# Kernel optimization log

Measured on AMD Instinct MI355X. Metric: run time of the kernel, lower is better.

## Reference

```python
import jax, jax.numpy as jnp
import numpy as np

EMB_DIM = 768
HEADS = 12
HEAD_DIM = EMB_DIM // HEADS  # 64


def setup_inputs() -> dict:
    key = jax.random.key(0)
    ks = jax.random.split(key, 9)
    s = 1.0 / np.sqrt(EMB_DIM)
    d = dict(
        x=jax.random.normal(ks[0], (2, 2048, EMB_DIM), dtype=jnp.float32),
        wq_w=jax.random.normal(ks[1], (EMB_DIM, EMB_DIM), dtype=jnp.float32) * s,
        wq_b=jax.random.normal(ks[2], (EMB_DIM,), dtype=jnp.float32) * 0.01,
        wk_w=jax.random.normal(ks[3], (EMB_DIM, EMB_DIM), dtype=jnp.float32) * s,
        wk_b=jax.random.normal(ks[4], (EMB_DIM,), dtype=jnp.float32) * 0.01,
        wv_w=jax.random.normal(ks[5], (EMB_DIM, EMB_DIM), dtype=jnp.float32) * s,
        wv_b=jax.random.normal(ks[6], (EMB_DIM,), dtype=jnp.float32) * 0.01,
        wo_w=jax.random.normal(ks[7], (EMB_DIM, EMB_DIM), dtype=jnp.float32) * s,
        wo_b=jax.random.normal(ks[8], (EMB_DIM,), dtype=jnp.float32) * 0.01,
    )
    return d


def reference(x, wq_w, wq_b, wk_w, wk_b, wv_w, wv_b, wo_w, wo_b):
    b, n, _ = x.shape
    # Linear projections (torch Linear: x @ W^T + b). q scaled by 1/8 == 1/sqrt(head_dim).
    q = (x @ wq_w.T + wq_b) / 8.0
    k = x @ wk_w.T + wk_b
    v = x @ wv_w.T + wv_b
    # [b, h, n, d]
    q = q.reshape(b, n, HEADS, HEAD_DIM).transpose(0, 2, 1, 3)
    k = k.reshape(b, n, HEADS, HEAD_DIM).transpose(0, 2, 1, 3)
    v = v.reshape(b, n, HEADS, HEAD_DIM).transpose(0, 2, 1, 3)
    # Full [b, h, n, n] score matrix with causal mask (strict upper triangle = -inf)
    scores = jnp.einsum('bhqd,bhkd->bhqk', q, k)
    causal = jnp.tril(jnp.ones((n, n), dtype=bool))  # True where allowed
    scores = jnp.where(causal[None, None], scores, -jnp.inf)
    attn = jax.nn.softmax(scores, axis=-1)
    out = jnp.einsum('bhqk,bhkd->bhqd', attn, v)
    out = out.transpose(0, 2, 1, 3).reshape(b, n, EMB_DIM)
    return out @ wo_w.T + wo_b
```

## Files before the change

kernel.cpp:

```cpp
#include <hip/hip_runtime.h>
#include <hip/hip_bf16.h>
#include <math.h>

#define EMB  768
#define NH   12
#define HD   64
#define SEQ  2048
#define BATCH 2
#define NTOK 4096

typedef __attribute__((ext_vector_type(8))) short short8;
typedef __attribute__((ext_vector_type(4))) float float4v;

static __device__ __forceinline__ short f2bf(float f) {
    __hip_bfloat16 h = __float2bfloat16(f);
    return *reinterpret_cast<short*>(&h);
}

static __device__ __forceinline__ void gll16(const void* g, void* l) {
    __builtin_amdgcn_global_load_lds(
        (const __attribute__((address_space(1))) void*)g,
        (__attribute__((address_space(3))) void*)l, 16, 0, 0);
}

__global__ __launch_bounds__(256) void cast_kernel(
    const float* __restrict__ x,  const float* __restrict__ wq,
    const float* __restrict__ wk, const float* __restrict__ wv,
    const float* __restrict__ wo,
    __hip_bfloat16* __restrict__ xb,  __hip_bfloat16* __restrict__ wqb,
    __hip_bfloat16* __restrict__ wkb, __hip_bfloat16* __restrict__ wvb,
    __hip_bfloat16* __restrict__ wob)
{
    const size_t S0 = (size_t)NTOK * EMB;
    const size_t S1 = (size_t)EMB * EMB;
    size_t i = ((size_t)blockIdx.x * 256 + threadIdx.x) * 8;
    const float* src; __hip_bfloat16* dst; size_t off;
    if      (i < S0)            { src = x;  dst = xb;  off = i; }
    else if (i < S0 + S1)       { src = wq; dst = wqb; off = i - S0; }
    else if (i < S0 + 2 * S1)   { src = wk; dst = wkb; off = i - S0 - S1; }
    else if (i < S0 + 3 * S1)   { src = wv; dst = wvb; off = i - S0 - 2 * S1; }
    else                        { src = wo; dst = wob; off = i - S0 - 3 * S1; }
    float4 f0 = *(const float4*)&src[off];
    float4 f1 = *(const float4*)&src[off + 4];
    short8 o;
    o[0] = f2bf(f0.x); o[1] = f2bf(f0.y); o[2] = f2bf(f0.z); o[3] = f2bf(f0.w);
    o[4] = f2bf(f1.x); o[5] = f2bf(f1.y); o[6] = f2bf(f1.z); o[7] = f2bf(f1.w);
    *(short8*)&dst[off] = o;
}

__global__ __launch_bounds__(256) void qkv_mfma_kernel(
    const __hip_bfloat16* __restrict__ xb,
    const __hip_bfloat16* __restrict__ wqb, const float* __restrict__ bq,
    const __hip_bfloat16* __restrict__ wkb, const float* __restrict__ bk,
    const __hip_bfloat16* __restrict__ wvb, const float* __restrict__ bv,
    __hip_bfloat16* __restrict__ q, __hip_bfloat16* __restrict__ k,
    __hip_bfloat16* __restrict__ vT)
{
    __shared__ __align__(16) short SM[16384];
    short* As = SM;
    short* Bs = SM + 8192;
    const int t = threadIdx.x;
    const int w = t >> 6, lane = t & 63;
    const int col = lane & 15, quad = lane >> 4;
    const int wm = w >> 1, wn = w & 1;
    const int m0 = blockIdx.y * 128;
    const int mat = blockIdx.x / 6;
    const int jj0 = (blockIdx.x % 6) * 128;
    const short* X = (const short*)xb;
    const short* W = (const short*)((mat == 0) ? wqb : (mat == 1) ? wkb : wvb);
    const float* bias = (mat == 0) ? bq : (mat == 1) ? bk : bv;

    float4v acc[4][4];
    #pragma unroll
    for (int mi = 0; mi < 4; ++mi)
        #pragma unroll
        for (int ni = 0; ni < 4; ++ni) acc[mi][ni] = (float4v){0.f, 0.f, 0.f, 0.f};

    for (int kb = 0; kb < EMB; kb += 64) {
        #pragma unroll
        for (int c = 0; c < 4; ++c) {
            int I = w * 256 + c * 64 + lane;
            int row = I >> 3;
            int c8 = (I & 7) ^ (row & 7);
            gll16(X + (size_t)(m0 + row) * EMB + kb + c8 * 8,
                  &As[(w * 256 + c * 64) * 8]);
            gll16(W + (size_t)(jj0 + row) * EMB + kb + c8 * 8,
                  &Bs[(w * 256 + c * 64) * 8]);
        }
        __syncthreads();
        #pragma unroll
        for (int ks = 0; ks < 2; ++ks) {
            short8 a[4], b[4];
            #pragma unroll
            for (int mi = 0; mi < 4; ++mi) {
                int row = wm * 64 + mi * 16 + col;
                a[mi] = *(short8*)&As[row * 64 + (((ks * 4 + quad) ^ (row & 7)) * 8)];
            }
            #pragma unroll
            for (int ni = 0; ni < 4; ++ni) {
                int row = wn * 64 + ni * 16 + col;
                b[ni] = *(short8*)&Bs[row * 64 + (((ks * 4 + quad) ^ (row & 7)) * 8)];
            }
            #pragma unroll
            for (int mi = 0; mi < 4; ++mi)
                #pragma unroll
                for (int ni = 0; ni < 4; ++ni)
                    acc[mi][ni] = __builtin_amdgcn_mfma_f32_16x16x32_bf16(
                        a[mi], b[ni], acc[mi][ni], 0, 0, 0);
        }
        __syncthreads();
    }
    const int bi = m0 >> 11, n0g = m0 & (SEQ - 1);
    if (mat != 2) {
        const float scale = (mat == 0) ? 0.125f : 1.0f;
        __hip_bfloat16* dstqk = (mat == 0) ? q : k;
        #pragma unroll
        for (int mi = 0; mi < 4; ++mi) {
            #pragma unroll
            for (int ni = 0; ni < 4; ++ni) {
                int gj = jj0 + wn * 64 + ni * 16 + col;
                int h = gj >> 6, d = gj & 63;
                float bsv = bias[gj];
                #pragma unroll
                for (int r = 0; r < 4; ++r) {
                    int gm = m0 + wm * 64 + mi * 16 + quad * 4 + r;
                    int bb = gm >> 11, n = gm & (SEQ - 1);
                    dstqk[(((size_t)bb * NH + h) * SEQ + n) * HD + d] =
                        __float2bfloat16((acc[mi][ni][r] + bsv) * scale);
                }
            }
        }
    } else {
        #pragma unroll
        for (int mi = 0; mi < 4; ++mi)
            #pragma unroll
            for (int ni = 0; ni < 4; ++ni) {
                int d_l = wn * 64 + ni * 16 + col;
                float bsv = bias[jj0 + d_l];
                #pragma unroll
                for (int r = 0; r < 4; ++r) {
                    int n_l = wm * 64 + mi * 16 + quad * 4 + r;
                    SM[(d_l << 7) + ((((n_l >> 3) ^ col) << 3) | (n_l & 7))] =
                        f2bf(acc[mi][ni][r] + bsv);
                }
            }
        __syncthreads();
        #pragma unroll
        for (int it = 0; it < 8; ++it) {
            int I = it * 256 + t;
            int d_l = I >> 4, c8 = I & 15;
            short8 val = *(short8*)&SM[(d_l << 7) + (c8 << 3)];
            int n_l = (c8 ^ (d_l & 15)) << 3;
            int gj = jj0 + d_l;
            int h = gj >> 6, dd = gj & 63;
            *(short8*)&vT[(((size_t)bi * NH + h) * HD + dd) * SEQ + n0g + n_l] = val;
        }
    }
}

__global__ __launch_bounds__(128) void attn_mfma_kernel(
    const __hip_bfloat16* __restrict__ qg, const __hip_bfloat16* __restrict__ kg,
    const __hip_bfloat16* __restrict__ vTg, __hip_bfloat16* __restrict__ ao,
    float* __restrict__ Os0, float* __restrict__ Os1,
    float* __restrict__ l0, float* __restrict__ l1)
{
    __shared__ __align__(16) short Ks[2][64 * 64];
    __shared__ __align__(16) short Vt[2][64 * 64];
    __shared__ __align__(16) short Ps[2][32][72];
    const int t = threadIdx.x;
    const int w = t >> 6, lane = t & 63;
    const int col = lane & 15, quad = lane >> 4;
    const int id = blockIdx.x;
    const int bh = id % 24;
    const int x = id / 24;
    int qt, c;
    if (x < 16) { qt = 16 + x; c = 0; }
    else {
        int i = x - 16, j = i >> 1;
        if ((i & 1) == 0) { qt = 31 - j; c = 1; }
        else              { qt = 15 - j; c = 0; }
    }
    const int kt0 = c * 16;
    const int ktend = (kt0 + 16 < qt + 1) ? kt0 + 16 : qt + 1;
    const int niter = ktend - kt0;
    const bool single = (qt <= 15);
    const int q0 = qt * 64;
    const size_t base = (size_t)bh * SEQ * HD;
    const short* kp = (const short*)kg + base;
    const short* vp = (const short*)vTg + base;
    const short* qp = (const short*)qg + base;

    short8 qa[2][2];
    #pragma unroll
    for (int mi = 0; mi < 2; ++mi) {
        int qrow = q0 + w * 32 + mi * 16 + col;
        #pragma unroll
        for (int ks = 0; ks < 2; ++ks)
            qa[mi][ks] = *(const short8*)&qp[(size_t)qrow * HD + ks * 32 + quad * 8];
    }
    float4v accO[2][4];
    float lacc[2][4];
    #pragma unroll
    for (int mi = 0; mi < 2; ++mi) {
        #pragma unroll
        for (int di = 0; di < 4; ++di) accO[mi][di] = (float4v){0.f, 0.f, 0.f, 0.f};
        #pragma unroll
        for (int r = 0; r < 4; ++r) lacc[mi][r] = 0.f;
    }

    {
        const int k0 = kt0 * 64;
        #pragma unroll
        for (int cc = 0; cc < 4; ++cc) {
            int I = w * 256 + cc * 64 + lane;
            int row = I >> 3;
            int c8 = (I & 7) ^ (row & 7);
            gll16(kp + (size_t)(k0 + row) * HD + c8 * 8, &Ks[0][(w * 256 + cc * 64) * 8]);
            gll16(vp + (size_t)row * SEQ + k0 + c8 * 8, &Vt[0][(w * 256 + cc * 64) * 8]);
        }
    }

    for (int lk = 0; lk < niter; ++lk) {
        const int kt = kt0 + lk;
        const int cur = lk & 1;
        const int k0 = kt * 64;
        __syncthreads();
        if (lk + 1 < niter) {
            const int kn = k0 + 64;
            #pragma unroll
            for (int cc = 0; cc < 4; ++cc) {
                int I = w * 256 + cc * 64 + lane;
                int row = I >> 3;
                int c8 = (I & 7) ^ (row & 7);
                gll16(kp + (size_t)(kn + row) * HD + c8 * 8,
                      &Ks[cur ^ 1][(w * 256 + cc * 64) * 8]);
                gll16(vp + (size_t)row * SEQ + kn + c8 * 8,
                      &Vt[cur ^ 1][(w * 256 + cc * 64) * 8]);
            }
        }
        const short* Kc = &Ks[cur][0];
        const short* Vc = &Vt[cur][0];

        float4v s[2][4];
        #pragma unroll
        for (int mi = 0; mi < 2; ++mi)
            #pragma unroll
            for (int ni = 0; ni < 4; ++ni) s[mi][ni] = (float4v){0.f, 0.f, 0.f, 0.f};
        #pragma unroll
        for (int ks = 0; ks < 2; ++ks)
            #pragma unroll
            for (int ni = 0; ni < 4; ++ni) {
                int row = ni * 16 + col;
                short8 kf = *(short8*)&Kc[row * 64 + (((ks * 4 + quad) ^ (row & 7)) * 8)];
                #pragma unroll
                for (int mi = 0; mi < 2; ++mi)
                    s[mi][ni] = __builtin_amdgcn_mfma_f32_16x16x32_bf16(
                        qa[mi][ks], kf, s[mi][ni], 0, 0, 0);
            }

        if (kt == qt) {
            #pragma unroll
            for (int mi = 0; mi < 2; ++mi)
                #pragma unroll
                for (int ni = 0; ni < 4; ++ni) {
                    int gcol = k0 + ni * 16 + col;
                    #pragma unroll
                    for (int r = 0; r < 4; ++r) {
                        int grow = q0 + w * 32 + mi * 16 + quad * 4 + r;
                        s[mi][ni][r] = (gcol > grow) ? 0.f : __expf(s[mi][ni][r]);
                    }
                }
        } else {
            #pragma unroll
            for (int mi = 0; mi < 2; ++mi)
                #pragma unroll
                for (int ni = 0; ni < 4; ++ni)
                    #pragma unroll
                    for (int r = 0; r < 4; ++r)
                        s[mi][ni][r] = __expf(s[mi][ni][r]);
        }
        #pragma unroll
        for (int mi = 0; mi < 2; ++mi)
            #pragma unroll
            for (int r = 0; r < 4; ++r)
                lacc[mi][r] += (s[mi][0][r] + s[mi][1][r]) + (s[mi][2][r] + s[mi][3][r]);

        #pragma unroll
        for (int mi = 0; mi < 2; ++mi)
            #pragma unroll
            for (int ni = 0; ni < 4; ++ni)
                #pragma unroll
                for (int r = 0; r < 4; ++r)
                    Ps[w][mi * 16 + quad * 4 + r][ni * 16 + col] = f2bf(s[mi][ni][r]);
        short8 pa[2][2];
        #pragma unroll
        for (int mi = 0; mi < 2; ++mi)
            #pragma unroll
            for (int ks = 0; ks < 2; ++ks)
                pa[mi][ks] = *(short8*)&Ps[w][mi * 16 + col][ks * 32 + quad * 8];

        #pragma unroll
        for (int ks = 0; ks < 2; ++ks)
            #pragma unroll
            for (int di = 0; di < 4; ++di) {
                int row = di * 16 + col;
                short8 vf = *(short8*)&Vc[row * 64 + (((ks * 4 + quad) ^ (row & 7)) * 8)];
                #pragma unroll
                for (int mi = 0; mi < 2; ++mi)
                    accO[mi][di] = __builtin_amdgcn_mfma_f32_16x16x32_bf16(
                        pa[mi][ks], vf, accO[mi][di], 0, 0, 0);
            }
    }

    #pragma unroll
    for (int msk = 1; msk < 16; msk <<= 1)
        #pragma unroll
        for (int mi = 0; mi < 2; ++mi)
            #pragma unroll
            for (int r = 0; r < 4; ++r)
                lacc[mi][r] += __shfl_xor(lacc[mi][r], msk);

    const int bi = bh / NH, h = bh % NH;
    if (single) {
        #pragma unroll
        for (int mi = 0; mi < 2; ++mi)
            #pragma unroll
            for (int r = 0; r < 4; ++r) {
                float inv = 1.0f / lacc[mi][r];
                int n = q0 + w * 32 + mi * 16 + quad * 4 + r;
                #pragma unroll
                for (int di = 0; di < 4; ++di)
                    ao[((size_t)bi * SEQ + n) * EMB + h * HD + di * 16 + col] =
                        __float2bfloat16(accO[mi][di][r] * inv);
            }
    } else {
        float* Os = c ? Os1 : Os0;
        float* ls = c ? l1 : l0;
        #pragma unroll
        for (int mi = 0; mi < 2; ++mi)
            #pragma unroll
            for (int r = 0; r < 4; ++r) {
                int n = q0 + w * 32 + mi * 16 + quad * 4 + r;
                int nn = n - 1024;
                size_t rowb = ((size_t)bi * 1024 + nn) * EMB + h * HD;
                #pragma unroll
                for (int di = 0; di < 4; ++di)
                    Os[rowb + di * 16 + col] = accO[mi][di][r];
                if (col == 0)
                    ls[((size_t)bi * 1024 + nn) * NH + h] = lacc[mi][r];
            }
    }
}

__global__ __launch_bounds__(256) void combine_kernel(
    const float* __restrict__ Os0, const float* __restrict__ Os1,
    const float* __restrict__ l0, const float* __restrict__ l1,
    __hip_bfloat16* __restrict__ ao)
{
    size_t e8 = ((size_t)blockIdx.x * 256 + threadIdx.x) * 8;
    int u = e8 / EMB;
    int within = e8 % EMB;
    int h = within >> 6;
    int bi = u >> 10, nn = u & 1023;
    float inv = 1.0f / (l0[(size_t)u * NH + h] + l1[(size_t)u * NH + h]);
    float4 a0 = *(const float4*)&Os0[e8];
    float4 a1 = *(const float4*)&Os0[e8 + 4];
    float4 b0 = *(const float4*)&Os1[e8];
    float4 b1 = *(const float4*)&Os1[e8 + 4];
    short8 o;
    o[0] = f2bf((a0.x + b0.x) * inv); o[1] = f2bf((a0.y + b0.y) * inv);
    o[2] = f2bf((a0.z + b0.z) * inv); o[3] = f2bf((a0.w + b0.w) * inv);
    o[4] = f2bf((a1.x + b1.x) * inv); o[5] = f2bf((a1.y + b1.y) * inv);
    o[6] = f2bf((a1.z + b1.z) * inv); o[7] = f2bf((a1.w + b1.w) * inv);
    *(short8*)&ao[((size_t)bi * SEQ + 1024 + nn) * EMB + within] = o;
}

__global__ __launch_bounds__(256) void out_proj_mfma_kernel(
    const __hip_bfloat16* __restrict__ a, const __hip_bfloat16* __restrict__ wob,
    const float* __restrict__ bias, float* __restrict__ out)
{
    __shared__ __align__(16) short As[64 * 64];
    __shared__ __align__(16) short Bs[128 * 64];
    const int t = threadIdx.x;
    const int w = t >> 6, lane = t & 63;
    const int col = lane & 15, quad = lane >> 4;
    const int m0 = blockIdx.y * 64;
    const int n0 = blockIdx.x * 128;
    const short* A = (const short*)a;
    const short* W = (const short*)wob;

    float4v acc[4][2];
    #pragma unroll
    for (int mi = 0; mi < 4; ++mi)
        #pragma unroll
        for (int ni = 0; ni < 2; ++ni) acc[mi][ni] = (float4v){0.f, 0.f, 0.f, 0.f};

    for (int kb = 0; kb < EMB; kb += 64) {
        #pragma unroll
        for (int c = 0; c < 2; ++c) {
            int I = w * 128 + c * 64 + lane;
            int row = I >> 3;
            int c8 = (I & 7) ^ (row & 7);
            gll16(A + (size_t)(m0 + row) * EMB + kb + c8 * 8,
                  &As[(w * 128 + c * 64) * 8]);
        }
        #pragma unroll
        for (int c = 0; c < 4; ++c) {
            int I = w * 256 + c * 64 + lane;
            int row = I >> 3;
            int c8 = (I & 7) ^ (row & 7);
            gll16(W + (size_t)(n0 + row) * EMB + kb + c8 * 8,
                  &Bs[(w * 256 + c * 64) * 8]);
        }
        __syncthreads();
        #pragma unroll
        for (int ks = 0; ks < 2; ++ks) {
            short8 av[4], bv[2];
            #pragma unroll
            for (int mi = 0; mi < 4; ++mi) {
                int row = mi * 16 + col;
                av[mi] = *(short8*)&As[row * 64 + (((ks * 4 + quad) ^ (row & 7)) * 8)];
            }
            #pragma unroll
            for (int ni = 0; ni < 2; ++ni) {
                int row = w * 32 + ni * 16 + col;
                bv[ni] = *(short8*)&Bs[row * 64 + (((ks * 4 + quad) ^ (row & 7)) * 8)];
            }
            #pragma unroll
            for (int mi = 0; mi < 4; ++mi)
                #pragma unroll
                for (int ni = 0; ni < 2; ++ni)
                    acc[mi][ni] = __builtin_amdgcn_mfma_f32_16x16x32_bf16(
                        av[mi], bv[ni], acc[mi][ni], 0, 0, 0);
        }
        __syncthreads();
    }
    #pragma unroll
    for (int mi = 0; mi < 4; ++mi)
        #pragma unroll
        for (int ni = 0; ni < 2; ++ni) {
            int gj = n0 + w * 32 + ni * 16 + col;
            float bsv = bias[gj];
            #pragma unroll
            for (int r = 0; r < 4; ++r) {
                int gm = m0 + mi * 16 + quad * 4 + r;
                out[(size_t)gm * EMB + gj] = acc[mi][ni][r] + bsv;
            }
        }
}

extern "C" void kernel_launch(void* const* d_in, const int* in_sizes, int n_in,
                              void* d_out, int out_size, void* d_ws, size_t ws_size,
                              hipStream_t stream) {
    const float* x  = (const float*)d_in[0];
    const float* wq = (const float*)d_in[1];
    const float* bq = (const float*)d_in[2];
    const float* wk = (const float*)d_in[3];
    const float* bk = (const float*)d_in[4];
    const float* wv = (const float*)d_in[5];
    const float* bv = (const float*)d_in[6];
    const float* wo = (const float*)d_in[7];
    const float* bo = (const float*)d_in[8];
    float* out = (float*)d_out;

    const size_t TOK = (size_t)NTOK * EMB;
    const size_t WSZ = (size_t)EMB * EMB;
    __hip_bfloat16* xb  = (__hip_bfloat16*)d_ws;
    __hip_bfloat16* wqb = xb  + TOK;
    __hip_bfloat16* wkb = wqb + WSZ;
    __hip_bfloat16* wvb = wkb + WSZ;
    __hip_bfloat16* wob = wvb + WSZ;
    __hip_bfloat16* qb  = wob + WSZ;
    __hip_bfloat16* kb  = qb  + TOK;
    __hip_bfloat16* vTb = kb  + TOK;
    __hip_bfloat16* aob = vTb + TOK;
    float* Os0 = (float*)d_ws;
    float* Os1 = (float*)(aob + TOK);
    float* l0  = Os1 + (size_t)2 * 1024 * EMB;
    float* l1  = l0  + (size_t)2 * 1024 * NH;

    cast_kernel<<<2688, 256, 0, stream>>>(x, wq, wk, wv, wo, xb, wqb, wkb, wvb, wob);
    qkv_mfma_kernel<<<dim3(18, 32), 256, 0, stream>>>(xb, wqb, bq, wkb, bk, wvb, bv,
                                                      qb, kb, vTb);
    attn_mfma_kernel<<<1152, 128, 0, stream>>>(qb, kb, vTb, aob, Os0, Os1, l0, l1);
    combine_kernel<<<768, 256, 0, stream>>>(Os0, Os1, l0, l1, aob);
    out_proj_mfma_kernel<<<dim3(6, 64), 256, 0, stream>>>(aob, wob, bo, out);
}
```

Before: 172.0 us.

## Use 128-row query tiles with four waves and fold log2e into Q scale

The attention kernel moves from 64-row query tiles with 2 waves to 128-row tiles with 4 waves, halving the grid. Each K/V tile loaded into shared memory is now reused by twice as many query rows, which cuts global and LDS load traffic per unit of work. The softmax scale now includes log2(e) in the Q projection so exp2f can replace __expf. The trade-offs are fewer blocks to balance across CUs and masking over two diagonal key tiles per query block.

```diff
diff --git a/kernel.cpp b/kernel.cpp
--- a/kernel.cpp
+++ b/kernel.cpp
@@ -112,7 +112,7 @@
     }
     const int bi = m0 >> 11, n0g = m0 & (SEQ - 1);
     if (mat != 2) {
-        const float scale = (mat == 0) ? 0.125f : 1.0f;
+        const float scale = (mat == 0) ? 0.125f * 1.44269504088896f : 1.0f;
         __hip_bfloat16* dstqk = (mat == 0) ? q : k;
         #pragma unroll
         for (int mi = 0; mi < 4; ++mi) {
@@ -158,7 +158,7 @@
     }
 }
 
-__global__ __launch_bounds__(128) void attn_mfma_kernel(
+__global__ __launch_bounds__(256) void attn_mfma_kernel(
     const __hip_bfloat16* __restrict__ qg, const __hip_bfloat16* __restrict__ kg,
     const __hip_bfloat16* __restrict__ vTg, __hip_bfloat16* __restrict__ ao,
     float* __restrict__ Os0, float* __restrict__ Os1,
@@ -166,25 +166,25 @@
 {
     __shared__ __align__(16) short Ks[2][64 * 64];
     __shared__ __align__(16) short Vt[2][64 * 64];
-    __shared__ __align__(16) short Ps[2][32][72];
+    __shared__ __align__(16) short Ps[4][32][72];
     const int t = threadIdx.x;
     const int w = t >> 6, lane = t & 63;
     const int col = lane & 15, quad = lane >> 4;
     const int id = blockIdx.x;
     const int bh = id % 24;
     const int x = id / 24;
-    int qt, c;
-    if (x < 16) { qt = 16 + x; c = 0; }
+    int b, c;
+    if (x < 8) { b = 8 + x; c = 0; }
     else {
-        int i = x - 16, j = i >> 1;
-        if ((i & 1) == 0) { qt = 31 - j; c = 1; }
-        else              { qt = 15 - j; c = 0; }
+        int i = x - 8, j = i >> 1;
+        if ((i & 1) == 0) { b = 7 - j;  c = 0; }
+        else              { b = 15 - j; c = 1; }
     }
     const int kt0 = c * 16;
-    const int ktend = (kt0 + 16 < qt + 1) ? kt0 + 16 : qt + 1;
+    const int ktend = (kt0 + 16 < 2 * b + 2) ? kt0 + 16 : 2 * b + 2;
     const int niter = ktend - kt0;
-    const bool single = (qt <= 15);
-    const int q0 = qt * 64;
+    const bool single = (b <= 7);
+    const int q0 = b * 128;
     const size_t base = (size_t)bh * SEQ * HD;
     const short* kp = (const short*)kg + base;
     const short* vp = (const short*)vTg + base;
@@ -193,7 +193,7 @@
     short8 qa[2][2];
     #pragma unroll
     for (int mi = 0; mi < 2; ++mi) {
-        int qrow = q0 + w * 32 + mi * 16 + col;
+        int qrow = q0 + (2 * w + mi) * 16 + col;
         #pragma unroll
         for (int ks = 0; ks < 2; ++ks)
             qa[mi][ks] = *(const short8*)&qp[(size_t)qrow * HD + ks * 32 + quad * 8];
@@ -211,12 +211,12 @@
     {
         const int k0 = kt0 * 64;
         #pragma unroll
-        for (int cc = 0; cc < 4; ++cc) {
-            int I = w * 256 + cc * 64 + lane;
+        for (int cc = 0; cc < 2; ++cc) {
+            int I = w * 128 + cc * 64 + lane;
             int row = I >> 3;
             int c8 = (I & 7) ^ (row & 7);
-            gll16(kp + (size_t)(k0 + row) * HD + c8 * 8, &Ks[0][(w * 256 + cc * 64) * 8]);
-            gll16(vp + (size_t)row * SEQ + k0 + c8 * 8, &Vt[0][(w * 256 + cc * 64) * 8]);
+            gll16(kp + (size_t)(k0 + row) * HD + c8 * 8, &Ks[0][(w * 128 + cc * 64) * 8]);
+            gll16(vp + (size_t)row * SEQ + k0 + c8 * 8, &Vt[0][(w * 128 + cc * 64) * 8]);
         }
     }
 
@@ -228,14 +228,14 @@
         if (lk + 1 < niter) {
             const int kn = k0 + 64;
             #pragma unroll
-            for (int cc = 0; cc < 4; ++cc) {
-                int I = w * 256 + cc * 64 + lane;
+            for (int cc = 0; cc < 2; ++cc) {
+                int I = w * 128 + cc * 64 + lane;
                 int row = I >> 3;
                 int c8 = (I & 7) ^ (row & 7);
                 gll16(kp + (size_t)(kn + row) * HD + c8 * 8,
-                      &Ks[cur ^ 1][(w * 256 + cc * 64) * 8]);
+                      &Ks[cur ^ 1][(w * 128 + cc * 64) * 8]);
                 gll16(vp + (size_t)row * SEQ + kn + c8 * 8,
-                      &Vt[cur ^ 1][(w * 256 + cc * 64) * 8]);
+                      &Vt[cur ^ 1][(w * 128 + cc * 64) * 8]);
             }
         }
         const short* Kc = &Ks[cur][0];
@@ -258,7 +258,7 @@
                         qa[mi][ks], kf, s[mi][ni], 0, 0, 0);
             }
 
-        if (kt == qt) {
+        if (k0 >= q0) {
             #pragma unroll
             for (int mi = 0; mi < 2; ++mi)
                 #pragma unroll
@@ -266,8 +266,8 @@
                     int gcol = k0 + ni * 16 + col;
                     #pragma unroll
                     for (int r = 0; r < 4; ++r) {
-                        int grow = q0 + w * 32 + mi * 16 + quad * 4 + r;
-                        s[mi][ni][r] = (gcol > grow) ? 0.f : __expf(s[mi][ni][r]);
+                        int grow = q0 + (2 * w + mi) * 16 + quad * 4 + r;
+                        s[mi][ni][r] = (gcol > grow) ? 0.f : exp2f(s[mi][ni][r]);
                     }
                 }
         } else {
@@ -277,7 +277,7 @@
                 for (int ni = 0; ni < 4; ++ni)
                     #pragma unroll
                     for (int r = 0; r < 4; ++r)
-                        s[mi][ni][r] = __expf(s[mi][ni][r]);
+                        s[mi][ni][r] = exp2f(s[mi][ni][r]);
         }
         #pragma unroll
         for (int mi = 0; mi < 2; ++mi)
@@ -327,7 +327,7 @@
             #pragma unroll
             for (int r = 0; r < 4; ++r) {
                 float inv = 1.0f / lacc[mi][r];
-                int n = q0 + w * 32 + mi * 16 + quad * 4 + r;
+                int n = q0 + (2 * w + mi) * 16 + quad * 4 + r;
                 #pragma unroll
                 for (int di = 0; di < 4; ++di)
                     ao[((size_t)bi * SEQ + n) * EMB + h * HD + di * 16 + col] =
@@ -340,7 +340,7 @@
         for (int mi = 0; mi < 2; ++mi)
             #pragma unroll
             for (int r = 0; r < 4; ++r) {
-                int n = q0 + w * 32 + mi * 16 + quad * 4 + r;
+                int n = q0 + (2 * w + mi) * 16 + quad * 4 + r;
                 int nn = n - 1024;
                 size_t rowb = ((size_t)bi * 1024 + nn) * EMB + h * HD;
                 #pragma unroll
@@ -482,7 +482,7 @@
     cast_kernel<<<2688, 256, 0, stream>>>(x, wq, wk, wv, wo, xb, wqb, wkb, wvb, wob);
     qkv_mfma_kernel<<<dim3(18, 32), 256, 0, stream>>>(xb, wqb, bq, wkb, bk, wvb, bv,
                                                       qb, kb, vTb);
-    attn_mfma_kernel<<<1152, 128, 0, stream>>>(qb, kb, vTb, aob, Os0, Os1, l0, l1);
+    attn_mfma_kernel<<<576, 256, 0, stream>>>(qb, kb, vTb, aob, Os0, Os1, l0, l1);
     combine_kernel<<<768, 256, 0, stream>>>(Os0, Os1, l0, l1, aob);
     out_proj_mfma_kernel<<<dim3(6, 64), 256, 0, stream>>>(aob, wob, bo, out);
 }
```

New measurement: 172.2 us. About the same (+0.2%).
